# Performance work log

Hardware: AMD Instinct MI355X
Metric: run time of the kernel (lower is better)

Reference implementation:

```python
import jax, jax.numpy as jnp
import numpy as np

N = 4096      # num_nodes
DIN = 16      # num_inputs
C = 16        # comm_channels
CHQ = 8       # ch_q
K = 10        # value-iteration steps
GAMMA = 0.99
EPS = float(np.finfo(np.float32).eps)


def setup_inputs() -> dict:
    key = jax.random.key(0)
    ks = jax.random.split(key, 8)
    x = jax.random.normal(ks[0], (N, DIN), dtype=jnp.float32)
    comms = jnp.zeros((N, C), dtype=jnp.float32)  # fresh comm state (reset())
    # random symmetric 0/1 adjacency, ~20 avg degree, zero diagonal
    u = jax.random.uniform(ks[1], (N, N), dtype=jnp.float32)
    a = (u < 0.005).astype(jnp.float32)
    adj = jnp.maximum(a, a.T) * (1.0 - jnp.eye(N, dtype=jnp.float32))
    mask = jnp.ones((N,), dtype=jnp.float32)
    # parameters (torch Linear: y = x @ W + b, weights stored [in, out] here)
    Wr = jax.random.normal(ks[2], (DIN + C, 1), dtype=jnp.float32) * 0.1   # reward_encoding
    br = jnp.zeros((1,), dtype=jnp.float32)
    We = jax.random.normal(ks[3], (DIN + C, CHQ), dtype=jnp.float32) * 0.1  # encoder
    be = jnp.zeros((CHQ,), dtype=jnp.float32)
    w_emb = jax.random.normal(ks[4], (CHQ,), dtype=jnp.float32) * 0.1       # embedder (ch_q -> 1)
    b_emb = jnp.zeros((), dtype=jnp.float32)
    Wa = jax.random.normal(ks[5], (CHQ,), dtype=jnp.float32) * 0.1          # action_decoding (1 -> ch_q)
    ba = jnp.zeros((CHQ,), dtype=jnp.float32)
    return dict(x=x, comms=comms, adj=adj, mask=mask, Wr=Wr, br=br,
                We=We, be=be, w_emb=w_emb, b_emb=b_emb, Wa=Wa, ba=ba, k=K)


def reference(x, comms, adj, mask, Wr, br, We, be, w_emb, b_emb, Wa, ba, k):
    n = adj.shape[0]
    # initialize_adj: symmetric normalization D^{-1/2} (A + I) D^{-1/2}
    a_norm = adj + jnp.eye(n, dtype=adj.dtype)
    deg = a_norm.sum(axis=0)
    dinv_sqrt = jnp.sqrt(1.0 / (deg + EPS))
    k3 = a_norm * dinv_sqrt[:, None] * dinv_sqrt[None, :]

    xc = jnp.concatenate([x, comms], axis=1)          # [n, DIN+C]
    r = (xc @ Wr + br)[:, 0]                          # reward per node [n]
    # embedder(cols - rows) fused: score[i,j] = s[j] - s[i] + b_emb
    s = (xc @ We + be) @ w_emb                        # [n]
    kernel3 = k3 * (s[None, :] - s[:, None] + b_emb)  # [n, n]

    # k-step value iteration
    v = jnp.zeros_like(r)
    for _ in range(k):
        k3v = kernel3 @ (r + GAMMA * v)               # [n]
        q = k3v[:, None] * Wa[None, :] + ba           # action_decoding (1 -> ch_q): [n, ch_q]
        v = q.max(axis=-1)                            # [n]

    # final_feature_process (rl=False): additive -inf mask
    return v + jnp.where(mask == 0, -jnp.inf, 0.0)
```

## Files before the change

kernel.cpp:

```cpp
#include <hip/hip_runtime.h>
#include <math.h>

#define NN     4096
#define NB     256
#define TPB    1024
#define WPB    16
#define CAP    128
#define SLOT   80
#define NB2    32
#define NPB2   128
#define MAXE   10
#define GAMMA  0.99f
#define EPSF   1.1920929e-07f
#define KSTEPS 10
#define RELSTR 16


__device__ __forceinline__ unsigned long long pk2(float lo, float hi) {
    return ((unsigned long long)__float_as_uint(hi) << 32) |
            (unsigned long long)__float_as_uint(lo);
}
__device__ __forceinline__ float lo_f(unsigned long long z) {
    return __uint_as_float((unsigned int)z);
}
__device__ __forceinline__ float hi_f(unsigned long long z) {
    return __uint_as_float((unsigned int)(z >> 32));
}

__device__ __forceinline__ void grid_barrier32(int* arr, int* rel, int k) {
    __syncthreads();
    if (threadIdx.x == 0)
        __hip_atomic_store(arr + blockIdx.x, k, __ATOMIC_RELAXED,
                           __HIP_MEMORY_SCOPE_AGENT);
    if (blockIdx.x == 0) {
        if (threadIdx.x < 64) {
            for (;;) {
                int a = k;
                if (threadIdx.x < NB2)
                    a = __hip_atomic_load(arr + threadIdx.x, __ATOMIC_RELAXED,
                                          __HIP_MEMORY_SCOPE_AGENT);
                if (__all(a >= k)) break;
                __builtin_amdgcn_s_sleep(1);
            }
            if (threadIdx.x < NB2)
                __hip_atomic_store(rel + (size_t)threadIdx.x * RELSTR, k,
                                   __ATOMIC_RELAXED, __HIP_MEMORY_SCOPE_AGENT);
        }
    } else if (threadIdx.x == 0) {
        while (__hip_atomic_load(rel + (size_t)blockIdx.x * RELSTR,
                                 __ATOMIC_RELAXED, __HIP_MEMORY_SCOPE_AGENT) < k)
            __builtin_amdgcn_s_sleep(1);
    }
    __syncthreads();
}

__global__ void __launch_bounds__(TPB) gvin_retire(
    const float* __restrict__ adj,  const float* __restrict__ x,
    const float* __restrict__ comms,const float* __restrict__ mask,
    const float* __restrict__ Wr,   const float* __restrict__ br,
    const float* __restrict__ We,   const float* __restrict__ be,
    const float* __restrict__ w_emb,const float* __restrict__ b_emb,
    const float* __restrict__ Wa,   const float* __restrict__ ba,
    int* arr, int* rel,
    unsigned long long* PD, unsigned long long* RS,
    float* UF0, float* UF1, int* CNT, int* CSRG,
    float* __restrict__ out)
{
    __shared__ int nbr[WPB][CAP];
    __shared__ int lcnt[WPB];
    __shared__ unsigned long long PDL[NN];
    __shared__ float UL[NN];
    const int tid  = (int)threadIdx.x;
    const int wave = tid >> 6;
    const int lane = tid & 63;
    const int g = (int)blockIdx.x * WPB + wave;

    if (lane == 0) { lcnt[wave] = 1; nbr[wave][0] = g; }

    const float4* rowp = (const float4*)(adj + (size_t)g * NN);
#pragma unroll 4
    for (int it = 0; it < 16; ++it) {
        const float4 v = rowp[lane + it * 64];
        const int b4 = (lane + it * 64) * 4;
        if (v.x != 0.0f) { int sl = atomicAdd(&lcnt[wave], 1); if (sl < CAP) nbr[wave][sl] = b4;     }
        if (v.y != 0.0f) { int sl = atomicAdd(&lcnt[wave], 1); if (sl < CAP) nbr[wave][sl] = b4 + 1; }
        if (v.z != 0.0f) { int sl = atomicAdd(&lcnt[wave], 1); if (sl < CAP) nbr[wave][sl] = b4 + 2; }
        if (v.w != 0.0f) { int sl = atomicAdd(&lcnt[wave], 1); if (sl < CAP) nbr[wave][sl] = b4 + 3; }
    }

    float pr = 0.0f, ps = 0.0f;
    if (lane < 32) {
        const float xc = (lane < 16) ? x[g * 16 + lane] : comms[g * 16 + (lane - 16)];
        float we = 0.0f;
#pragma unroll
        for (int c = 0; c < 8; ++c) we += We[lane * 8 + c] * w_emb[c];
        pr = xc * Wr[lane];
        ps = xc * we;
    } else if (lane == 32) {
#pragma unroll
        for (int c = 0; c < 8; ++c) ps += be[c] * w_emb[c];
        pr = br[0];
    }
#pragma unroll
    for (int off = 32; off; off >>= 1) { pr += __shfl_xor(pr, off); ps += __shfl_xor(ps, off); }
    const float r = pr, s = ps;

    const int   deg  = lcnt[wave];
    const int   cl   = deg < CAP ? deg : CAP;
    const int   clp  = cl < SLOT ? cl : SLOT;
    const float dinv = sqrtf(1.0f / ((float)deg + EPSF));
    const float p    = dinv * (s + b_emb[0]);

    if (lane == 0) {
        __hip_atomic_store(PD  + g, pk2(p, dinv), __ATOMIC_RELAXED, __HIP_MEMORY_SCOPE_AGENT);
        __hip_atomic_store(RS  + g, pk2(r, s),    __ATOMIC_RELAXED, __HIP_MEMORY_SCOPE_AGENT);
        __hip_atomic_store(UF0 + g, r,            __ATOMIC_RELAXED, __HIP_MEMORY_SCOPE_AGENT);
        __hip_atomic_store(CNT + g, clp,          __ATOMIC_RELAXED, __HIP_MEMORY_SCOPE_AGENT);
    }
    if (lane < clp)
        __hip_atomic_store(CSRG + g * SLOT + lane, nbr[wave][lane],
                           __ATOMIC_RELAXED, __HIP_MEMORY_SCOPE_AGENT);
    if (64 + lane < clp)
        __hip_atomic_store(CSRG + g * SLOT + 64 + lane, nbr[wave][64 + lane],
                           __ATOMIC_RELAXED, __HIP_MEMORY_SCOPE_AGENT);

    __syncthreads();
    if (tid == 0)
        __hip_atomic_store(arr + blockIdx.x, 1, __ATOMIC_RELAXED, __HIP_MEMORY_SCOPE_AGENT);
    if (blockIdx.x >= NB2) return;
    if (blockIdx.x == 0) {
        if (tid < 64) {
            const int base = tid * 4;
            for (;;) {
                const int a0 = __hip_atomic_load(arr + base + 0, __ATOMIC_RELAXED, __HIP_MEMORY_SCOPE_AGENT);
                const int a1 = __hip_atomic_load(arr + base + 1, __ATOMIC_RELAXED, __HIP_MEMORY_SCOPE_AGENT);
                const int a2 = __hip_atomic_load(arr + base + 2, __ATOMIC_RELAXED, __HIP_MEMORY_SCOPE_AGENT);
                const int a3 = __hip_atomic_load(arr + base + 3, __ATOMIC_RELAXED, __HIP_MEMORY_SCOPE_AGENT);
                if (__all((a0 >= 1) && (a1 >= 1) && (a2 >= 1) && (a3 >= 1))) break;
                __builtin_amdgcn_s_sleep(1);
            }
            if (tid < NB2)
                __hip_atomic_store(rel + (size_t)tid * RELSTR, 1,
                                   __ATOMIC_RELAXED, __HIP_MEMORY_SCOPE_AGENT);
        }
    } else if (tid == 0) {
        while (__hip_atomic_load(rel + (size_t)blockIdx.x * RELSTR,
                                 __ATOMIC_RELAXED, __HIP_MEMORY_SCOPE_AGENT) < 1)
            __builtin_amdgcn_s_sleep(1);
    }
    __syncthreads();

    {
        unsigned long long w0, w1, w2, w3;
        asm volatile(
            "global_load_dwordx2 %0, %4, off sc1\n\t"
            "global_load_dwordx2 %1, %5, off sc1\n\t"
            "global_load_dwordx2 %2, %6, off sc1\n\t"
            "global_load_dwordx2 %3, %7, off sc1\n\t"
            "s_waitcnt vmcnt(0)"
            : "=&v"(w0), "=&v"(w1), "=&v"(w2), "=&v"(w3)
            : "v"(PD + tid), "v"(PD + tid + 1024),
              "v"(PD + tid + 2048), "v"(PD + tid + 3072)
            : "memory");
        PDL[tid] = w0; PDL[tid + 1024] = w1;
        PDL[tid + 2048] = w2; PDL[tid + 3072] = w3;
    }
    __syncthreads();

    const int q   = tid >> 3, sub = tid & 7;
    const int n   = (int)blockIdx.x * NPB2 + q;
    const int dgn = __hip_atomic_load(CNT + n, __ATOMIC_RELAXED, __HIP_MEMORY_SCOPE_AGENT);
    int jj[MAXE]; float pe[MAXE], de[MAXE];
#pragma unroll
    for (int e = 0; e < MAXE; ++e) {
        const int k  = sub + (e << 3);
        const bool vv = k < dgn;
        const int idx = n * SLOT + (vv ? k : 0);
        const int j   = __hip_atomic_load(CSRG + idx, __ATOMIC_RELAXED, __HIP_MEMORY_SCOPE_AGENT);
        jj[e] = vv ? j : 0;
        const unsigned long long z = PDL[jj[e]];
        pe[e] = vv ? lo_f(z) : 0.0f;
        de[e] = vv ? hi_f(z) : 0.0f;
    }
    float rn = 0.0f, sn = 0.0f, dvn = 0.0f;
    if (sub == 0) {
        const unsigned long long z = __hip_atomic_load(RS + n, __ATOMIC_RELAXED, __HIP_MEMORY_SCOPE_AGENT);
        rn = lo_f(z); sn = hi_f(z); dvn = hi_f(PDL[n]);
    }
    float wa[8], bb[8];
#pragma unroll
    for (int c = 0; c < 8; ++c) { wa[c] = Wa[c]; bb[c] = ba[c]; }

    float v = 0.0f;
    for (int t = 0; t < KSTEPS; ++t) {
        const float* Uf = (t & 1) ? UF1 : UF0;
        float*       Uo = (t & 1) ? UF0 : UF1;
        {
            float f0, f1, f2, f3;
            asm volatile(
                "global_load_dword %0, %4, off sc1\n\t"
                "global_load_dword %1, %5, off sc1\n\t"
                "global_load_dword %2, %6, off sc1\n\t"
                "global_load_dword %3, %7, off sc1\n\t"
                "s_waitcnt vmcnt(0)"
                : "=&v"(f0), "=&v"(f1), "=&v"(f2), "=&v"(f3)
                : "v"(Uf + tid), "v"(Uf + tid + 1024),
                  "v"(Uf + tid + 2048), "v"(Uf + tid + 3072)
                : "memory");
            UL[tid] = f0; UL[tid + 1024] = f1;
            UL[tid + 2048] = f2; UL[tid + 3072] = f3;
        }
        __syncthreads();

        float a1 = 0.0f, a2 = 0.0f;
#pragma unroll
        for (int e = 0; e < MAXE; ++e) {
            const float u = UL[jj[e]];
            a1 = fmaf(pe[e], u, a1);
            a2 = fmaf(de[e], u, a2);
        }
        a1 += __shfl_xor(a1, 1); a2 += __shfl_xor(a2, 1);
        a1 += __shfl_xor(a1, 2); a2 += __shfl_xor(a2, 2);
        a1 += __shfl_xor(a1, 4); a2 += __shfl_xor(a2, 4);

        if (sub == 0) {
            const float k3v = dvn * (a1 - sn * a2);
            v = fmaf(k3v, wa[0], bb[0]);
#pragma unroll
            for (int c = 1; c < 8; ++c) v = fmaxf(v, fmaf(k3v, wa[c], bb[c]));
            if (t < KSTEPS - 1)
                __hip_atomic_store(Uo + n, rn + GAMMA * v,
                                   __ATOMIC_RELAXED, __HIP_MEMORY_SCOPE_AGENT);
        }
        if (t < KSTEPS - 1)
            grid_barrier32(arr, rel, t + 2);
    }

    if (sub == 0) out[n] = v + (mask[n] == 0.0f ? -INFINITY : 0.0f);
}

extern "C" void kernel_launch(void* const* d_in, const int* in_sizes, int n_in,
                              void* d_out, int out_size, void* d_ws, size_t ws_size,
                              hipStream_t stream) {
    const float* x     = (const float*)d_in[0];
    const float* comms = (const float*)d_in[1];
    const float* adj   = (const float*)d_in[2];
    const float* mask  = (const float*)d_in[3];
    const float* Wr    = (const float*)d_in[4];
    const float* br    = (const float*)d_in[5];
    const float* We    = (const float*)d_in[6];
    const float* be    = (const float*)d_in[7];
    const float* w_emb = (const float*)d_in[8];
    const float* b_emb = (const float*)d_in[9];
    const float* Wa    = (const float*)d_in[10];
    const float* ba    = (const float*)d_in[11];

    char* ws = (char*)d_ws;
    size_t off = 0;
    int* arr               = (int*)(ws + off); off += 4096;
    int* rel               = (int*)(ws + off); off += 4096;
    unsigned long long* PD = (unsigned long long*)(ws + off); off += (size_t)NN * 8;
    unsigned long long* RS = (unsigned long long*)(ws + off); off += (size_t)NN * 8;
    float* UF0             = (float*)(ws + off); off += (size_t)NN * 4;
    float* UF1             = (float*)(ws + off); off += (size_t)NN * 4;
    int* CNT               = (int*)(ws + off); off += (size_t)NN * 4;
    int* CSRG              = (int*)(ws + off); off += (size_t)NN * SLOT * 4;
    float* out = (float*)d_out;

    gvin_retire<<<dim3(NB), dim3(TPB), 0, stream>>>(
        adj, x, comms, mask, Wr, br, We, be, w_emb, b_emb, Wa, ba,
        arr, rel, PD, RS, UF0, UF1, CNT, CSRG, out);
}
```

Baseline: 153.4 us.

## Replace per-step grid barrier with tagged dataflow synchronization on value buffers

Each value-iteration step no longer ends with a centralized grid barrier across the 32 persistent blocks. Instead, every published value is packed with a step tag into a 64-bit word, and consumers re-poll only the neighbor entries whose tag is stale. This removes barrier round-trip latency and lets blocks proceed as soon as their own inputs are ready. In exchange, the per-step snapshot load and shared-memory staging double in size, and stale entries add polling traffic to global memory. Double-buffering with tags also relies on a producer never getting two steps ahead of a slow reader.

```diff
diff --git a/kernel.cpp b/kernel.cpp
--- a/kernel.cpp
+++ b/kernel.cpp
@@ -26,35 +26,15 @@
 __device__ __forceinline__ float hi_f(unsigned long long z) {
     return __uint_as_float((unsigned int)(z >> 32));
 }
-
-__device__ __forceinline__ void grid_barrier32(int* arr, int* rel, int k) {
-    __syncthreads();
-    if (threadIdx.x == 0)
-        __hip_atomic_store(arr + blockIdx.x, k, __ATOMIC_RELAXED,
-                           __HIP_MEMORY_SCOPE_AGENT);
-    if (blockIdx.x == 0) {
-        if (threadIdx.x < 64) {
-            for (;;) {
-                int a = k;
-                if (threadIdx.x < NB2)
-                    a = __hip_atomic_load(arr + threadIdx.x, __ATOMIC_RELAXED,
-                                          __HIP_MEMORY_SCOPE_AGENT);
-                if (__all(a >= k)) break;
-                __builtin_amdgcn_s_sleep(1);
-            }
-            if (threadIdx.x < NB2)
-                __hip_atomic_store(rel + (size_t)threadIdx.x * RELSTR, k,
-                                   __ATOMIC_RELAXED, __HIP_MEMORY_SCOPE_AGENT);
-        }
-    } else if (threadIdx.x == 0) {
-        while (__hip_atomic_load(rel + (size_t)blockIdx.x * RELSTR,
-                                 __ATOMIC_RELAXED, __HIP_MEMORY_SCOPE_AGENT) < k)
-            __builtin_amdgcn_s_sleep(1);
-    }
-    __syncthreads();
-}
-
-__global__ void __launch_bounds__(TPB) gvin_retire(
+__device__ __forceinline__ unsigned long long pkVT(float v, int tag) {
+    return ((unsigned long long)(unsigned int)tag << 32) |
+            (unsigned long long)__float_as_uint(v);
+}
+__device__ __forceinline__ int tag_of(unsigned long long z) {
+    return (int)(unsigned int)(z >> 32);
+}
+
+__global__ void __launch_bounds__(TPB) gvin_flow32(
     const float* __restrict__ adj,  const float* __restrict__ x,
     const float* __restrict__ comms,const float* __restrict__ mask,
     const float* __restrict__ Wr,   const float* __restrict__ br,
@@ -63,13 +43,13 @@
     const float* __restrict__ Wa,   const float* __restrict__ ba,
     int* arr, int* rel,
     unsigned long long* PD, unsigned long long* RS,
-    float* UF0, float* UF1, int* CNT, int* CSRG,
+    unsigned long long* UT0, unsigned long long* UT1, int* CNT, int* CSRG,
     float* __restrict__ out)
 {
     __shared__ int nbr[WPB][CAP];
     __shared__ int lcnt[WPB];
     __shared__ unsigned long long PDL[NN];
-    __shared__ float UL[NN];
+    __shared__ unsigned long long UL[NN];
     const int tid  = (int)threadIdx.x;
     const int wave = tid >> 6;
     const int lane = tid & 63;
@@ -114,7 +94,7 @@
     if (lane == 0) {
         __hip_atomic_store(PD  + g, pk2(p, dinv), __ATOMIC_RELAXED, __HIP_MEMORY_SCOPE_AGENT);
         __hip_atomic_store(RS  + g, pk2(r, s),    __ATOMIC_RELAXED, __HIP_MEMORY_SCOPE_AGENT);
-        __hip_atomic_store(UF0 + g, r,            __ATOMIC_RELAXED, __HIP_MEMORY_SCOPE_AGENT);
+        __hip_atomic_store(UT0 + g, pkVT(r, 0),   __ATOMIC_RELAXED, __HIP_MEMORY_SCOPE_AGENT);
         __hip_atomic_store(CNT + g, clp,          __ATOMIC_RELAXED, __HIP_MEMORY_SCOPE_AGENT);
     }
     if (lane < clp)
@@ -193,31 +173,56 @@
 
     float v = 0.0f;
     for (int t = 0; t < KSTEPS; ++t) {
-        const float* Uf = (t & 1) ? UF1 : UF0;
-        float*       Uo = (t & 1) ? UF0 : UF1;
+        unsigned long long* Uin  = (t & 1) ? UT1 : UT0;
+        unsigned long long* Uout = (t & 1) ? UT0 : UT1;
+
+        __syncthreads();
         {
-            float f0, f1, f2, f3;
+            unsigned long long w0, w1, w2, w3;
             asm volatile(
-                "global_load_dword %0, %4, off sc1\n\t"
-                "global_load_dword %1, %5, off sc1\n\t"
-                "global_load_dword %2, %6, off sc1\n\t"
-                "global_load_dword %3, %7, off sc1\n\t"
+                "global_load_dwordx2 %0, %4, off sc1\n\t"
+                "global_load_dwordx2 %1, %5, off sc1\n\t"
+                "global_load_dwordx2 %2, %6, off sc1\n\t"
+                "global_load_dwordx2 %3, %7, off sc1\n\t"
                 "s_waitcnt vmcnt(0)"
-                : "=&v"(f0), "=&v"(f1), "=&v"(f2), "=&v"(f3)
-                : "v"(Uf + tid), "v"(Uf + tid + 1024),
-                  "v"(Uf + tid + 2048), "v"(Uf + tid + 3072)
+                : "=&v"(w0), "=&v"(w1), "=&v"(w2), "=&v"(w3)
+                : "v"(Uin + tid), "v"(Uin + tid + 1024),
+                  "v"(Uin + tid + 2048), "v"(Uin + tid + 3072)
                 : "memory");
-            UL[tid] = f0; UL[tid + 1024] = f1;
-            UL[tid + 2048] = f2; UL[tid + 3072] = f3;
+            UL[tid] = w0; UL[tid + 1024] = w1;
+            UL[tid + 2048] = w2; UL[tid + 3072] = w3;
         }
         __syncthreads();
 
+        float ue[MAXE]; bool st[MAXE];
+        bool need = false;
+#pragma unroll
+        for (int e = 0; e < MAXE; ++e) {
+            const unsigned long long z = UL[jj[e]];
+            ue[e] = lo_f(z);
+            const bool vv = (sub + (e << 3)) < dgn;
+            st[e] = vv && (tag_of(z) != t);
+            need |= st[e];
+        }
+        while (__any(need)) {
+            need = false;
+#pragma unroll
+            for (int e = 0; e < MAXE; ++e) {
+                if (st[e]) {
+                    const unsigned long long z = __hip_atomic_load(
+                        Uin + jj[e], __ATOMIC_RELAXED, __HIP_MEMORY_SCOPE_AGENT);
+                    if (tag_of(z) == t) { ue[e] = lo_f(z); st[e] = false; }
+                    else need = true;
+                }
+            }
+            if (need) __builtin_amdgcn_s_sleep(1);
+        }
+
         float a1 = 0.0f, a2 = 0.0f;
 #pragma unroll
         for (int e = 0; e < MAXE; ++e) {
-            const float u = UL[jj[e]];
-            a1 = fmaf(pe[e], u, a1);
-            a2 = fmaf(de[e], u, a2);
+            a1 = fmaf(pe[e], ue[e], a1);
+            a2 = fmaf(de[e], ue[e], a2);
         }
         a1 += __shfl_xor(a1, 1); a2 += __shfl_xor(a2, 1);
         a1 += __shfl_xor(a1, 2); a2 += __shfl_xor(a2, 2);
@@ -229,11 +234,9 @@
 #pragma unroll
             for (int c = 1; c < 8; ++c) v = fmaxf(v, fmaf(k3v, wa[c], bb[c]));
             if (t < KSTEPS - 1)
-                __hip_atomic_store(Uo + n, rn + GAMMA * v,
+                __hip_atomic_store(Uout + n, pkVT(rn + GAMMA * v, t + 1),
                                    __ATOMIC_RELAXED, __HIP_MEMORY_SCOPE_AGENT);
         }
-        if (t < KSTEPS - 1)
-            grid_barrier32(arr, rel, t + 2);
     }
 
     if (sub == 0) out[n] = v + (mask[n] == 0.0f ? -INFINITY : 0.0f);
@@ -257,17 +260,17 @@
 
     char* ws = (char*)d_ws;
     size_t off = 0;
-    int* arr               = (int*)(ws + off); off += 4096;
-    int* rel               = (int*)(ws + off); off += 4096;
-    unsigned long long* PD = (unsigned long long*)(ws + off); off += (size_t)NN * 8;
-    unsigned long long* RS = (unsigned long long*)(ws + off); off += (size_t)NN * 8;
-    float* UF0             = (float*)(ws + off); off += (size_t)NN * 4;
-    float* UF1             = (float*)(ws + off); off += (size_t)NN * 4;
-    int* CNT               = (int*)(ws + off); off += (size_t)NN * 4;
-    int* CSRG              = (int*)(ws + off); off += (size_t)NN * SLOT * 4;
+    int* arr                = (int*)(ws + off); off += 4096;
+    int* rel                = (int*)(ws + off); off += 4096;
+    unsigned long long* PD  = (unsigned long long*)(ws + off); off += (size_t)NN * 8;
+    unsigned long long* RS  = (unsigned long long*)(ws + off); off += (size_t)NN * 8;
+    unsigned long long* UT0 = (unsigned long long*)(ws + off); off += (size_t)NN * 8;
+    unsigned long long* UT1 = (unsigned long long*)(ws + off); off += (size_t)NN * 8;
+    int* CNT                = (int*)(ws + off); off += (size_t)NN * 4;
+    int* CSRG               = (int*)(ws + off); off += (size_t)NN * SLOT * 4;
     float* out = (float*)d_out;
 
-    gvin_retire<<<dim3(NB), dim3(TPB), 0, stream>>>(
+    gvin_flow32<<<dim3(NB), dim3(TPB), 0, stream>>>(
         adj, x, comms, mask, Wr, br, We, be, w_emb, b_emb, Wa, ba,
-        arr, rel, PD, RS, UF0, UF1, CNT, CSRG, out);
-}
+        arr, rel, PD, RS, UT0, UT1, CNT, CSRG, out);
+}
```

Measured after the change: 190.5 us. 1.24x slower.

## Replace centralized grid barrier with all-to-all per-block flag matrix

Applied to the files above, without the earlier changes.

Replaces the two-hop grid barrier used in the value-iteration loop with a flag matrix. In the old barrier every block arrived at block 0, which then released the others. Now each of the 32 active blocks writes its step counter into a dedicated padded slot for every peer, and each block spins on its own 32 incoming flags before loading the next value vector. This takes one round-trip of barrier latency off each of the nine iteration syncs, in exchange for more flag traffic and polling. The new flags are never reset inside the kernel, so repeated launches depend on the workspace being zeroed between calls.

```diff
diff --git a/kernel.cpp b/kernel.cpp
--- a/kernel.cpp
+++ b/kernel.cpp
@@ -27,41 +27,14 @@
     return __uint_as_float((unsigned int)(z >> 32));
 }
 
-__device__ __forceinline__ void grid_barrier32(int* arr, int* rel, int k) {
-    __syncthreads();
-    if (threadIdx.x == 0)
-        __hip_atomic_store(arr + blockIdx.x, k, __ATOMIC_RELAXED,
-                           __HIP_MEMORY_SCOPE_AGENT);
-    if (blockIdx.x == 0) {
-        if (threadIdx.x < 64) {
-            for (;;) {
-                int a = k;
-                if (threadIdx.x < NB2)
-                    a = __hip_atomic_load(arr + threadIdx.x, __ATOMIC_RELAXED,
-                                          __HIP_MEMORY_SCOPE_AGENT);
-                if (__all(a >= k)) break;
-                __builtin_amdgcn_s_sleep(1);
-            }
-            if (threadIdx.x < NB2)
-                __hip_atomic_store(rel + (size_t)threadIdx.x * RELSTR, k,
-                                   __ATOMIC_RELAXED, __HIP_MEMORY_SCOPE_AGENT);
-        }
-    } else if (threadIdx.x == 0) {
-        while (__hip_atomic_load(rel + (size_t)blockIdx.x * RELSTR,
-                                 __ATOMIC_RELAXED, __HIP_MEMORY_SCOPE_AGENT) < k)
-            __builtin_amdgcn_s_sleep(1);
-    }
-    __syncthreads();
-}
-
-__global__ void __launch_bounds__(TPB) gvin_retire(
+__global__ void __launch_bounds__(TPB) gvin_hop1(
     const float* __restrict__ adj,  const float* __restrict__ x,
     const float* __restrict__ comms,const float* __restrict__ mask,
     const float* __restrict__ Wr,   const float* __restrict__ br,
     const float* __restrict__ We,   const float* __restrict__ be,
     const float* __restrict__ w_emb,const float* __restrict__ b_emb,
     const float* __restrict__ Wa,   const float* __restrict__ ba,
-    int* arr, int* rel,
+    int* arr, int* rel, int* FL,
     unsigned long long* PD, unsigned long long* RS,
     float* UF0, float* UF1, int* CNT, int* CSRG,
     float* __restrict__ out)
@@ -195,6 +168,17 @@
     for (int t = 0; t < KSTEPS; ++t) {
         const float* Uf = (t & 1) ? UF1 : UF0;
         float*       Uo = (t & 1) ? UF0 : UF1;
+
+        if (t > 0) {
+            if (wave == 0 && lane < NB2) {
+                while (__hip_atomic_load(
+                           FL + ((size_t)blockIdx.x * NB2 + lane) * RELSTR,
+                           __ATOMIC_RELAXED, __HIP_MEMORY_SCOPE_AGENT) < t)
+                    __builtin_amdgcn_s_sleep(1);
+            }
+            __syncthreads();
+        }
+
         {
             float f0, f1, f2, f3;
             asm volatile(
@@ -232,8 +216,13 @@
                 __hip_atomic_store(Uo + n, rn + GAMMA * v,
                                    __ATOMIC_RELAXED, __HIP_MEMORY_SCOPE_AGENT);
         }
-        if (t < KSTEPS - 1)
-            grid_barrier32(arr, rel, t + 2);
+        if (t < KSTEPS - 1) {
+            __syncthreads();
+            if (tid < NB2)
+                __hip_atomic_store(
+                    FL + ((size_t)tid * NB2 + blockIdx.x) * RELSTR, t + 1,
+                    __ATOMIC_RELAXED, __HIP_MEMORY_SCOPE_AGENT);
+        }
     }
 
     if (sub == 0) out[n] = v + (mask[n] == 0.0f ? -INFINITY : 0.0f);
@@ -259,6 +248,7 @@
     size_t off = 0;
     int* arr               = (int*)(ws + off); off += 4096;
     int* rel               = (int*)(ws + off); off += 4096;
+    int* FL                = (int*)(ws + off); off += (size_t)NB2 * NB2 * 64;
     unsigned long long* PD = (unsigned long long*)(ws + off); off += (size_t)NN * 8;
     unsigned long long* RS = (unsigned long long*)(ws + off); off += (size_t)NN * 8;
     float* UF0             = (float*)(ws + off); off += (size_t)NN * 4;
@@ -267,7 +257,7 @@
     int* CSRG              = (int*)(ws + off); off += (size_t)NN * SLOT * 4;
     float* out = (float*)d_out;
 
-    gvin_retire<<<dim3(NB), dim3(TPB), 0, stream>>>(
+    gvin_hop1<<<dim3(NB), dim3(TPB), 0, stream>>>(
         adj, x, comms, mask, Wr, br, We, be, w_emb, b_emb, Wa, ba,
-        arr, rel, PD, RS, UF0, UF1, CNT, CSRG, out);
-}
+        arr, rel, FL, PD, RS, UF0, UF1, CNT, CSRG, out);
+}
```

Measured after the change: 147.9 us. -3.6%, faster.
